# Kernel tuning notes

Measured on AMD Instinct MI355X. Metric: run time of the kernel, lower is better.

Reference implementation:

```python
import jax, jax.numpy as jnp
import numpy as np

N = 50000   # nodes
E = 800000  # edges (before self-loops)
IN = 128; H = 4; C = 32; HC = H * C; OUT = 47
EPS = 1e-16  # PyG softmax denominator eps
NEG_SLOPE = 0.2


def setup_inputs() -> dict:
    key = jax.random.key(0)
    ks = jax.random.split(key, 20)
    g = lambda k, shape, s=0.1: (jax.random.normal(k, shape, dtype=jnp.float32) * s)
    inp = {}
    inp["x"] = jax.random.normal(ks[0], (N, IN), dtype=jnp.float32)
    inp["edge_index"] = jax.random.randint(ks[1], (2, E), 0, N, dtype=jnp.int32)
    # layer 0: GATConv(IN -> H*C, concat=True) + skip Linear(IN -> HC)
    inp["lin_w0"] = g(ks[2], (IN, HC)); inp["att_src0"] = g(ks[3], (H, C)); inp["att_dst0"] = g(ks[4], (H, C))
    inp["bias0"] = g(ks[5], (HC,)); inp["skip_w0"] = g(ks[6], (IN, HC)); inp["skip_b0"] = g(ks[7], (HC,))
    # layer 1: GATConv(HC -> H*C, concat=True) + skip Linear(HC -> HC)
    inp["lin_w1"] = g(ks[8], (HC, HC)); inp["att_src1"] = g(ks[9], (H, C)); inp["att_dst1"] = g(ks[10], (H, C))
    inp["bias1"] = g(ks[11], (HC,)); inp["skip_w1"] = g(ks[12], (HC, HC)); inp["skip_b1"] = g(ks[13], (HC,))
    # layer 2: GATConv(HC -> OUT, heads=H, concat=False) + skip Linear(HC -> OUT)
    inp["lin_w2"] = g(ks[14], (HC, H * OUT)); inp["att_src2"] = g(ks[15], (H, OUT)); inp["att_dst2"] = g(ks[16], (H, OUT))
    inp["bias2"] = g(ks[17], (OUT,)); inp["skip_w2"] = g(ks[18], (HC, OUT)); inp["skip_b2"] = g(ks[19], (OUT,))
    return inp


def _gat_conv(x, src, dst, lin_w, att_src, att_dst, bias, concat):
    """PyG GATConv (self-loops already appended to src/dst)."""
    h, c = att_src.shape
    n = x.shape[0]
    xh = (x @ lin_w).reshape(n, h, c)                      # [N, H, C]
    a_src = jnp.einsum('nhc,hc->nh', xh, att_src)          # [N, H]
    a_dst = jnp.einsum('nhc,hc->nh', xh, att_dst)          # [N, H]
    e = a_src[src] + a_dst[dst]                            # [E', H]
    e = jax.nn.leaky_relu(e, NEG_SLOPE)
    # segment softmax over incoming edges per destination node
    m = jax.ops.segment_max(e, dst, num_segments=n)        # [N, H]
    ex = jnp.exp(e - m[dst])
    s = jax.ops.segment_sum(ex, dst, num_segments=n)       # [N, H]
    alpha = ex / (s[dst] + EPS)                            # [E', H]
    out = jax.ops.segment_sum(xh[src] * alpha[:, :, None], dst, num_segments=n)  # [N, H, C]
    out = out.reshape(n, h * c) if concat else out.mean(axis=1)
    return out + bias


def reference(x, edge_index, lin_w0, att_src0, att_dst0, bias0, skip_w0, skip_b0,
              lin_w1, att_src1, att_dst1, bias1, skip_w1, skip_b1,
              lin_w2, att_src2, att_dst2, bias2, skip_w2, skip_b2):
    n = x.shape[0]
    loop = jnp.arange(n, dtype=edge_index.dtype)
    src = jnp.concatenate([edge_index[0], loop])
    dst = jnp.concatenate([edge_index[1], loop])
    # layer 0 (+ skip, ELU; dropout is identity at inference)
    x = _gat_conv(x, src, dst, lin_w0, att_src0, att_dst0, bias0, True) + x @ skip_w0 + skip_b0
    x = jax.nn.elu(x)
    # layer 1
    x = _gat_conv(x, src, dst, lin_w1, att_src1, att_dst1, bias1, True) + x @ skip_w1 + skip_b1
    x = jax.nn.elu(x)
    # layer 2 (concat=False -> head mean), no activation
    x = _gat_conv(x, src, dst, lin_w2, att_src2, att_dst2, bias2, False) + x @ skip_w2 + skip_b2
    return x
```

## Files before the change

### kernel.cpp

```cpp
#include <hip/hip_runtime.h>
#include <math.h>
#include <type_traits>

#define KD 128
#define HC 128
#define NF2 188
#define NF2PB 192
#define OUTC 47

typedef __attribute__((ext_vector_type(8))) __bf16 bf16x8;
typedef __attribute__((ext_vector_type(4))) float f32x4;
typedef __attribute__((ext_vector_type(2))) float f32x2;

#ifdef __has_builtin
#if __has_builtin(__builtin_amdgcn_cvt_pk_f32_fp8)
#define HAVE_CVT_FP8_DEC 1
#endif
#if __has_builtin(__builtin_amdgcn_cvt_pk_fp8_f32)
#define HAVE_CVT_FP8_ENC 1
#endif
#endif

__device__ inline float bfhi_to_f(unsigned int u) {
    union { unsigned int u; float f; } c; c.u = u & 0xFFFF0000u; return c.f;
}
__device__ inline float bflo_to_f(unsigned int u) {
    union { unsigned int u; float f; } c; c.u = u << 16; return c.f;
}
__device__ inline unsigned short f_to_bfu(float f) {
    return __builtin_bit_cast(unsigned short, (__bf16)f);
}
__device__ inline unsigned int pk_bf(float a, float b) {
    return (unsigned int)f_to_bfu(a) | ((unsigned int)f_to_bfu(b) << 16);
}

__device__ inline void dot2bf(float& acc, unsigned int x, unsigned int a) {
    asm("v_dot2_f32_bf16 %0, %1, %2, %0" : "+v"(acc) : "v"(x), "v"(a));
}
__device__ inline unsigned int permb(unsigned int hi, unsigned int lo, unsigned int sel) {
    return __builtin_amdgcn_perm(hi, lo, sel);
}

#ifndef HAVE_CVT_FP8_DEC
__device__ inline float fp8_to_f32_b(unsigned int b) {
    int e = (b >> 3) & 15, m = b & 7;
    float v = e ? ldexpf((float)(8 + m), e - 10) : ldexpf((float)m, -9);
    return (b & 0x80) ? -v : v;
}
#endif
__device__ inline void fp8x4_dec(unsigned int q, float& a, float& b, float& c, float& d) {
#ifdef HAVE_CVT_FP8_DEC
    f32x2 lo = __builtin_amdgcn_cvt_pk_f32_fp8((int)q, false);
    f32x2 hi = __builtin_amdgcn_cvt_pk_f32_fp8((int)q, true);
    a = lo[0]; b = lo[1]; c = hi[0]; d = hi[1];
#else
    a = fp8_to_f32_b(q & 0xFF); b = fp8_to_f32_b((q >> 8) & 0xFF);
    c = fp8_to_f32_b((q >> 16) & 0xFF); d = fp8_to_f32_b((q >> 24) & 0xFF);
#endif
}
__device__ inline unsigned char f32_to_fp8(float v) {
#ifdef HAVE_CVT_FP8_ENC
    return (unsigned char)(__builtin_amdgcn_cvt_pk_fp8_f32(v, v, 0, false) & 0xFF);
#else
    unsigned u = __builtin_bit_cast(unsigned, v);
    unsigned s = (u >> 24) & 0x80;
    float a = fabsf(v);
    if (a < 0.0009765625f) return (unsigned char)s;
    if (a >= 448.f) return (unsigned char)(s | 0x7E);
    int e; float m = frexpf(a, &e);
    int E = e - 1 + 7;
    int mi = (int)rintf(m * 16.f);
    if (mi == 16) { mi = 8; ++E; if (E >= 16) return (unsigned char)(s | 0x7E); }
    if (E <= 0) {
        int q = (int)rintf(a * 512.f); if (q > 7) q = 7;
        return (unsigned char)(s | q);
    }
    return (unsigned char)(s | (E << 3) | (mi - 8));
#endif
}
__device__ inline float fp8dot(unsigned int q, float4 al, float acc) {
    float a, b, c, d;
    fp8x4_dec(q, a, b, c, d);
    return acc + al.x * a + al.y * b + al.z * c + al.w * d;
}

__global__ void count_kernel(const int* __restrict__ dst, int* deg, int e) {
    int t = blockIdx.x * blockDim.x + threadIdx.x;
    int base = t * 2;
    if (base + 1 < e) {
        int2 d = *(const int2*)(dst + base);
        atomicAdd(&deg[d.x], 1); atomicAdd(&deg[d.y], 1);
    } else {
        for (int k = base; k < e; ++k) atomicAdd(&deg[dst[k]], 1);
    }
}

__global__ __launch_bounds__(256) void scan_base_kernel(
    int* __restrict__ deg, int* counter,
    int* __restrict__ row_ptr, int* __restrict__ fill, int* __restrict__ col, int n) {
    int i = blockIdx.x * 256 + threadIdx.x;
    int v = (i < n) ? (deg[i] + 1) : 0;
    int lane = threadIdx.x & 63, w = threadIdx.x >> 6;
    int incl = v;
#pragma unroll
    for (int off = 1; off < 64; off <<= 1) {
        int u = __shfl_up(incl, off, 64);
        if (lane >= off) incl += u;
    }
    __shared__ int wsum[4];
    __shared__ int base_sh;
    if (lane == 63) wsum[w] = incl;
    __syncthreads();
    if (threadIdx.x == 0)
        base_sh = atomicAdd(counter, wsum[0] + wsum[1] + wsum[2] + wsum[3]);
    int woff = 0;
    for (int k = 0; k < w; ++k) woff += wsum[k];
    __syncthreads();
    int excl = base_sh + woff + incl - v;
    if (i < n) {
        row_ptr[i] = excl;
        col[excl] = i;
        fill[i] = excl + 1;
        deg[i] = v;
    }
}

__global__ void fill_kernel(const int* __restrict__ ei, int* fill, int* col, int e) {
    int t = blockIdx.x * blockDim.x + threadIdx.x;
    int base = t * 2;
    if (base + 1 < e) {
        int2 s = *(const int2*)(ei + base);
        int2 d = *(const int2*)(ei + e + base);
        int p0 = atomicAdd(&fill[d.x], 1);
        int p1 = atomicAdd(&fill[d.y], 1);
        __builtin_nontemporal_store(s.x, &col[p0]);
        __builtin_nontemporal_store(s.y, &col[p1]);
    } else {
        for (int k = base; k < e; ++k) {
            int pos = atomicAdd(&fill[ei[e + k]], 1);
            __builtin_nontemporal_store(ei[k], &col[pos]);
        }
    }
}

__global__ __launch_bounds__(256) void prep_w_kernel(
    const float* __restrict__ lw0, const float* __restrict__ sw0,
    const float* __restrict__ lw1, const float* __restrict__ sw1,
    const float* __restrict__ lw2, const float* __restrict__ sw2,
    __bf16* __restrict__ bt) {
    int idx = blockIdx.x * 256 + threadIdx.x;
    int buf = idx >> 15;
    int r = idx & 32767;
    int n = r >> 7, k = r & 127;
    float v = 0.f;
    if (buf == 0) v = (n < 128) ? lw0[k * 128 + n] : sw0[k * 128 + n - 128];
    else if (buf == 1) v = (n < 128) ? lw1[k * 128 + n] : sw1[k * 128 + n - 128];
    else {
        if (n < 188) v = lw2[k * 188 + n];
        else if (n >= 192 && n < 239) v = sw2[k * 47 + n - 192];
    }
    bt[idx] = (__bf16)v;
}

template <typename AT, typename SKT, int NLIN, int NSK, int TR>
__global__ __launch_bounds__(256) void gemm_fused_kernel(
    const AT* __restrict__ A, const __bf16* __restrict__ Bt,
    void* __restrict__ out0, int N0, int ldc0,
    const float* __restrict__ bias1, SKT* __restrict__ out1, int N1, int M) {
    __shared__ __bf16 As[64][136];
    __shared__ __bf16 Bs[64][136];
    int tid = threadIdx.x;
    int m0 = blockIdx.x * 64;

#pragma unroll
    for (int rep = 0; rep < 4; ++rep) {
        int idx = tid + rep * 256;
        int row = idx >> 4, seg = idx & 15;
        int gm = m0 + row;
        bf16x8 v = {};
        if (gm < M) {
            if constexpr (std::is_same<AT, float>::value) {
                const float* p = A + gm * KD + seg * 8;
                float4 f0 = *(const float4*)p;
                float4 f1 = *(const float4*)(p + 4);
                v[0] = (__bf16)f0.x; v[1] = (__bf16)f0.y; v[2] = (__bf16)f0.z; v[3] = (__bf16)f0.w;
                v[4] = (__bf16)f1.x; v[5] = (__bf16)f1.y; v[6] = (__bf16)f1.z; v[7] = (__bf16)f1.w;
            } else {
                v = *(const bf16x8*)(A + gm * KD + seg * 8);
            }
        }
        *(bf16x8*)&As[row][seg * 8] = v;
    }
    __syncthreads();

    int w = tid >> 6, lane = tid & 63;
    int lr = lane & 15, quad = lane >> 4;

#pragma unroll
    for (int t = 0; t < NLIN + NSK; ++t) {
        bool second = t >= NLIN;
        int N = second ? N1 : N0;
        int n0 = (second ? (t - NLIN) : t) * 64;
        if (t) __syncthreads();
#pragma unroll
        for (int rep = 0; rep < 4; ++rep) {
            int idx = tid + rep * 256;
            int row = idx >> 4, seg = idx & 15;
            *(bf16x8*)&Bs[row][seg * 8] =
                *(const bf16x8*)(Bt + ((t * 64 + row) << 7) + seg * 8);
        }
        __syncthreads();

        f32x4 acc[4] = {};
#pragma unroll
        for (int kc = 0; kc < 128; kc += 32) {
            bf16x8 a0 = *(const bf16x8*)&As[w * 16 + lr][kc + quad * 8];
            bf16x8 b0 = *(const bf16x8*)&Bs[lr][kc + quad * 8];
            bf16x8 b1 = *(const bf16x8*)&Bs[16 + lr][kc + quad * 8];
            bf16x8 b2 = *(const bf16x8*)&Bs[32 + lr][kc + quad * 8];
            bf16x8 b3 = *(const bf16x8*)&Bs[48 + lr][kc + quad * 8];
            acc[0] = __builtin_amdgcn_mfma_f32_16x16x32_bf16(a0, b0, acc[0], 0, 0, 0);
            acc[1] = __builtin_amdgcn_mfma_f32_16x16x32_bf16(a0, b1, acc[1], 0, 0, 0);
            acc[2] = __builtin_amdgcn_mfma_f32_16x16x32_bf16(a0, b2, acc[2], 0, 0, 0);
            acc[3] = __builtin_amdgcn_mfma_f32_16x16x32_bf16(a0, b3, acc[3], 0, 0, 0);
        }
#pragma unroll
        for (int c = 0; c < 4; ++c) {
#pragma unroll
            for (int reg = 0; reg < 4; ++reg) {
                int row = m0 + w * 16 + quad * 4 + reg;
                int colg = n0 + c * 16 + lr;
                if (row < M && colg < N) {
                    float v = acc[c][reg];
                    if (second) {
                        v += bias1[colg];
                        out1[row * N + colg] = (SKT)v;
                    } else if (TR) {
                        int h = (colg * 1395) >> 16;
                        ((unsigned char*)out0)[row * ldc0 + (colg - 47 * h) * 4 + h] =
                            f32_to_fp8(v);
                    } else {
                        ((__bf16*)out0)[row * ldc0 + colg] = (__bf16)v;
                    }
                }
            }
        }
    }
}

__global__ __launch_bounds__(256) void att_kernel(
    const __bf16* __restrict__ xh, const float* __restrict__ att_s,
    const float* __restrict__ att_d, float* __restrict__ a_src,
    float* __restrict__ a_dst, int n) {
    int tid = blockIdx.x * 256 + threadIdx.x;
    int node = tid >> 4;
    int l16 = threadIdx.x & 15;
    if (node >= n) return;
    uint4 q = ((const uint4*)xh)[node * 16 + l16];
    int f0 = l16 * 8;
    float4 as0 = *(const float4*)(att_s + f0);
    float4 as1 = *(const float4*)(att_s + f0 + 4);
    float4 ad0 = *(const float4*)(att_d + f0);
    float4 ad1 = *(const float4*)(att_d + f0 + 4);
    float x0 = bflo_to_f(q.x), x1 = bfhi_to_f(q.x);
    float x2 = bflo_to_f(q.y), x3 = bfhi_to_f(q.y);
    float x4 = bflo_to_f(q.z), x5 = bfhi_to_f(q.z);
    float x6 = bflo_to_f(q.w), x7 = bfhi_to_f(q.w);
    float hs = x0 * as0.x + x1 * as0.y + x2 * as0.z + x3 * as0.w
             + x4 * as1.x + x5 * as1.y + x6 * as1.z + x7 * as1.w;
    float hd = x0 * ad0.x + x1 * ad0.y + x2 * ad0.z + x3 * ad0.w
             + x4 * ad1.x + x5 * ad1.y + x6 * ad1.z + x7 * ad1.w;
    hs += __shfl_xor(hs, 1, 64); hs += __shfl_xor(hs, 2, 64);
    hd += __shfl_xor(hd, 1, 64); hd += __shfl_xor(hd, 2, 64);
    if ((l16 & 3) == 0) {
        int h = l16 >> 2;
        a_src[node * 4 + h] = hs;
        a_dst[node * 4 + h] = hd;
    }
}

__global__ __launch_bounds__(256) void att2_kernel(
    const unsigned char* __restrict__ xh8, const float* __restrict__ att_s,
    const float* __restrict__ att_d, float* __restrict__ a_src,
    float* __restrict__ a_dst, int n) {
    int node = (blockIdx.x * 256 + threadIdx.x) >> 6;
    int lane = threadIdx.x & 63;
    if (node >= n) return;
    float ps0 = 0.f, ps1 = 0.f, ps2 = 0.f, ps3 = 0.f;
    float pd0 = 0.f, pd1 = 0.f, pd2 = 0.f, pd3 = 0.f;
    if (lane < 47) {
        unsigned int q = ((const unsigned int*)(xh8 + node * NF2PB))[lane];
        float x0, x1, x2, x3;
        fp8x4_dec(q, x0, x1, x2, x3);
        ps0 = x0 * att_s[lane];       ps1 = x1 * att_s[47 + lane];
        ps2 = x2 * att_s[94 + lane];  ps3 = x3 * att_s[141 + lane];
        pd0 = x0 * att_d[lane];       pd1 = x1 * att_d[47 + lane];
        pd2 = x2 * att_d[94 + lane];  pd3 = x3 * att_d[141 + lane];
    }
#pragma unroll
    for (int off = 1; off <= 32; off <<= 1) {
        ps0 += __shfl_xor(ps0, off, 64); ps1 += __shfl_xor(ps1, off, 64);
        ps2 += __shfl_xor(ps2, off, 64); ps3 += __shfl_xor(ps3, off, 64);
        pd0 += __shfl_xor(pd0, off, 64); pd1 += __shfl_xor(pd1, off, 64);
        pd2 += __shfl_xor(pd2, off, 64); pd3 += __shfl_xor(pd3, off, 64);
    }
    if (lane < 4) {
        float vs = (lane == 0) ? ps0 : (lane == 1) ? ps1 : (lane == 2) ? ps2 : ps3;
        float vd = (lane == 0) ? pd0 : (lane == 1) ? pd1 : (lane == 2) ? pd2 : pd3;
        a_src[node * 4 + lane] = vs;
        a_dst[node * 4 + lane] = vd;
    }
}

template <int MODE>
__global__ __launch_bounds__(256) void agg_kernel(
    const void* __restrict__ xhp, const float* __restrict__ a_src,
    const float* __restrict__ a_dst, const void* __restrict__ skipp,
    const float* __restrict__ bias, const int* __restrict__ row_ptr,
    const int* __restrict__ deg, const int* __restrict__ col,
    void* __restrict__ outp, int n) {
    __shared__ float s_af[4][64][4];
    __shared__ unsigned s_ap[4][32][4];
    __shared__ int s_j[4][64];
    int w = threadIdx.x >> 6;
    int lane = threadIdx.x & 63;
    int node = (blockIdx.x << 2) + w;
    bool active = node < n;
    int node_c = active ? node : 0;
    int start = row_ptr[node_c];
    int end = start + (active ? deg[node_c] : 0);
    float4 ad4 = *(const float4*)(a_dst + 4 * node_c);
    float adh[4] = {ad4.x, ad4.y, ad4.z, ad4.w};

    int e0 = start + lane;
    bool ok0 = e0 < end;
    int jcap = ok0 ? col[e0] : 0;
    float evc[4];
    {
        float4 as4 = *(const float4*)(a_src + 4 * jcap);
        float v0 = as4.x + adh[0]; v0 = v0 > 0.f ? v0 : 0.2f * v0;
        float v1 = as4.y + adh[1]; v1 = v1 > 0.f ? v1 : 0.2f * v1;
        float v2 = as4.z + adh[2]; v2 = v2 > 0.f ? v2 : 0.2f * v2;
        float v3 = as4.w + adh[3]; v3 = v3 > 0.f ? v3 : 0.2f * v3;
        evc[0] = ok0 ? __expf(v0) : 0.f;
        evc[1] = ok0 ? __expf(v1) : 0.f;
        evc[2] = ok0 ? __expf(v2) : 0.f;
        evc[3] = ok0 ? __expf(v3) : 0.f;
    }
    float s[4] = {evc[0], evc[1], evc[2], evc[3]};
    for (int e = e0 + 64; e < end; e += 64) {
        int j = col[e];
        float4 as4 = *(const float4*)(a_src + 4 * j);
        float ev[4] = {as4.x + adh[0], as4.y + adh[1], as4.z + adh[2], as4.w + adh[3]};
#pragma unroll
        for (int h = 0; h < 4; ++h) {
            float v = ev[h] > 0.f ? ev[h] : 0.2f * ev[h];
            s[h] += __expf(v);
        }
    }
#pragma unroll
    for (int off = 32; off >= 1; off >>= 1)
#pragma unroll
        for (int h = 0; h < 4; ++h) s[h] += __shfl_xor(s[h], off, 64);
    float inv[4];
#pragma unroll
    for (int h = 0; h < 4; ++h) inv[h] = 1.f / (s[h] + 1e-16f);

    int half = lane >> 5, fl = lane & 31, myh2 = fl >> 3;
    bool lv = lane < 47;
    float acc0 = 0.f, acc1 = 0.f, acc2 = 0.f, acc3 = 0.f;
    const uint2* xb2 = (const uint2*)xhp;
    const unsigned int* x8 = (const unsigned int*)xhp;

    auto run_chunk = [&](int cnt) {
        if constexpr (MODE == 0) {
            int npair = (cnt + 1) >> 1;
            int p = half;
            for (; p + 2 < npair; p += 4) {
                int2 j0 = *(const int2*)&s_j[w][2 * p];
                int2 j1 = *(const int2*)&s_j[w][2 * p + 4];
                unsigned ap0 = s_ap[w][p][myh2];
                unsigned ap1 = s_ap[w][p + 2][myh2];
                uint2 qa0 = xb2[(j0.x << 5) + fl];
                uint2 qb0 = xb2[(j0.y << 5) + fl];
                uint2 qa1 = xb2[(j1.x << 5) + fl];
                uint2 qb1 = xb2[(j1.y << 5) + fl];
                dot2bf(acc0, permb(qb0.x, qa0.x, 0x05040100u), ap0);
                dot2bf(acc1, permb(qb0.x, qa0.x, 0x07060302u), ap0);
                dot2bf(acc2, permb(qb0.y, qa0.y, 0x05040100u), ap0);
                dot2bf(acc3, permb(qb0.y, qa0.y, 0x07060302u), ap0);
                dot2bf(acc0, permb(qb1.x, qa1.x, 0x05040100u), ap1);
                dot2bf(acc1, permb(qb1.x, qa1.x, 0x07060302u), ap1);
                dot2bf(acc2, permb(qb1.y, qa1.y, 0x05040100u), ap1);
                dot2bf(acc3, permb(qb1.y, qa1.y, 0x07060302u), ap1);
            }
            for (; p < npair; p += 2) {
                int2 j0 = *(const int2*)&s_j[w][2 * p];
                unsigned ap0 = s_ap[w][p][myh2];
                uint2 qa0 = xb2[(j0.x << 5) + fl];
                uint2 qb0 = xb2[(j0.y << 5) + fl];
                dot2bf(acc0, permb(qb0.x, qa0.x, 0x05040100u), ap0);
                dot2bf(acc1, permb(qb0.x, qa0.x, 0x07060302u), ap0);
                dot2bf(acc2, permb(qb0.y, qa0.y, 0x05040100u), ap0);
                dot2bf(acc3, permb(qb0.y, qa0.y, 0x07060302u), ap0);
            }
        } else {
            int t = 0;
            for (; t + 7 < cnt; t += 8) {
                unsigned int q0 = lv ? x8[s_j[w][t] * 48 + lane] : 0u;
                unsigned int q1 = lv ? x8[s_j[w][t + 1] * 48 + lane] : 0u;
                unsigned int q2 = lv ? x8[s_j[w][t + 2] * 48 + lane] : 0u;
                unsigned int q3 = lv ? x8[s_j[w][t + 3] * 48 + lane] : 0u;
                unsigned int q4 = lv ? x8[s_j[w][t + 4] * 48 + lane] : 0u;
                unsigned int q5 = lv ? x8[s_j[w][t + 5] * 48 + lane] : 0u;
                unsigned int q6 = lv ? x8[s_j[w][t + 6] * 48 + lane] : 0u;
                unsigned int q7 = lv ? x8[s_j[w][t + 7] * 48 + lane] : 0u;
                acc0 = fp8dot(q0, *(const float4*)&s_af[w][t][0], acc0);
                acc0 = fp8dot(q1, *(const float4*)&s_af[w][t + 1][0], acc0);
                acc0 = fp8dot(q2, *(const float4*)&s_af[w][t + 2][0], acc0);
                acc0 = fp8dot(q3, *(const float4*)&s_af[w][t + 3][0], acc0);
                acc0 = fp8dot(q4, *(const float4*)&s_af[w][t + 4][0], acc0);
                acc0 = fp8dot(q5, *(const float4*)&s_af[w][t + 5][0], acc0);
                acc0 = fp8dot(q6, *(const float4*)&s_af[w][t + 6][0], acc0);
                acc0 = fp8dot(q7, *(const float4*)&s_af[w][t + 7][0], acc0);
            }
            for (; t + 3 < cnt; t += 4) {
                unsigned int q0 = lv ? x8[s_j[w][t] * 48 + lane] : 0u;
                unsigned int q1 = lv ? x8[s_j[w][t + 1] * 48 + lane] : 0u;
                unsigned int q2 = lv ? x8[s_j[w][t + 2] * 48 + lane] : 0u;
                unsigned int q3 = lv ? x8[s_j[w][t + 3] * 48 + lane] : 0u;
                acc0 = fp8dot(q0, *(const float4*)&s_af[w][t][0], acc0);
                acc0 = fp8dot(q1, *(const float4*)&s_af[w][t + 1][0], acc0);
                acc0 = fp8dot(q2, *(const float4*)&s_af[w][t + 2][0], acc0);
                acc0 = fp8dot(q3, *(const float4*)&s_af[w][t + 3][0], acc0);
            }
            for (; t < cnt; ++t) {
                unsigned int q = lv ? x8[s_j[w][t] * 48 + lane] : 0u;
                acc0 = fp8dot(q, *(const float4*)&s_af[w][t][0], acc0);
            }
        }
    };

    {
        float al[4];
#pragma unroll
        for (int h = 0; h < 4; ++h) al[h] = evc[h] * inv[h];
        s_j[w][lane] = jcap;
        if constexpr (MODE == 0) {
            float o0 = __shfl_xor(al[0], 1, 64);
            float o1 = __shfl_xor(al[1], 1, 64);
            float o2 = __shfl_xor(al[2], 1, 64);
            float o3 = __shfl_xor(al[3], 1, 64);
            if (!(lane & 1)) {
                uint4 pk = make_uint4(pk_bf(al[0], o0), pk_bf(al[1], o1),
                                      pk_bf(al[2], o2), pk_bf(al[3], o3));
                *(uint4*)&s_ap[w][lane >> 1][0] = pk;
            }
        } else {
            *(float4*)&s_af[w][lane][0] = make_float4(al[0], al[1], al[2], al[3]);
        }
        int cnt = end - start; if (cnt > 64) cnt = 64;
        run_chunk(cnt);
    }
    for (int base = start + 64; base < end; base += 64) {
        int e = base + lane;
        bool ok = e < end;
        int jv = ok ? col[e] : 0;
        float4 as4 = *(const float4*)(a_src + 4 * jv);
        float asv[4] = {as4.x, as4.y, as4.z, as4.w};
        float al[4];
#pragma unroll
        for (int h = 0; h < 4; ++h) {
            float ev = asv[h] + adh[h];
            ev = ev > 0.f ? ev : 0.2f * ev;
            al[h] = ok ? __expf(ev) * inv[h] : 0.f;
        }
        s_j[w][lane] = jv;
        if constexpr (MODE == 0) {
            float o0 = __shfl_xor(al[0], 1, 64);
            float o1 = __shfl_xor(al[1], 1, 64);
            float o2 = __shfl_xor(al[2], 1, 64);
            float o3 = __shfl_xor(al[3], 1, 64);
            if (!(lane & 1)) {
                uint4 pk = make_uint4(pk_bf(al[0], o0), pk_bf(al[1], o1),
                                      pk_bf(al[2], o2), pk_bf(al[3], o3));
                *(uint4*)&s_ap[w][lane >> 1][0] = pk;
            }
        } else {
            *(float4*)&s_af[w][lane][0] = make_float4(al[0], al[1], al[2], al[3]);
        }
        int cnt = end - base; if (cnt > 64) cnt = 64;
        run_chunk(cnt);
    }

    if constexpr (MODE == 0) {
        acc0 += __shfl_xor(acc0, 32, 64);
        acc1 += __shfl_xor(acc1, 32, 64);
        acc2 += __shfl_xor(acc2, 32, 64);
        acc3 += __shfl_xor(acc3, 32, 64);
        if (active && half == 0) {
            float4 bb = *(const float4*)(bias + 4 * fl);
            uint2 skq = ((const uint2*)skipp)[(node << 5) + fl];
            float v0 = acc0 + bb.x + bflo_to_f(skq.x);
            float v1 = acc1 + bb.y + bfhi_to_f(skq.x);
            float v2 = acc2 + bb.z + bflo_to_f(skq.y);
            float v3 = acc3 + bb.w + bfhi_to_f(skq.y);
            v0 = v0 > 0.f ? v0 : (__expf(v0) - 1.f);
            v1 = v1 > 0.f ? v1 : (__expf(v1) - 1.f);
            v2 = v2 > 0.f ? v2 : (__expf(v2) - 1.f);
            v3 = v3 > 0.f ? v3 : (__expf(v3) - 1.f);
            uint2 o = make_uint2(pk_bf(v0, v1), pk_bf(v2, v3));
            ((uint2*)outp)[(node << 5) + fl] = o;
        }
    } else {
        if (active && lane < OUTC) {
            const float* skip = (const float*)skipp;
            float v = acc0 * 0.25f + bias[lane] + skip[node * OUTC + lane];
            ((float*)outp)[node * OUTC + lane] = v;
        }
    }
}

extern "C" void kernel_launch(void* const* d_in, const int* in_sizes, int n_in,
                              void* d_out, int out_size, void* d_ws, size_t ws_size,
                              hipStream_t stream) {
    const float* x        = (const float*)d_in[0];
    const int*   ei       = (const int*)d_in[1];
    const float* lin_w0   = (const float*)d_in[2];
    const float* att_src0 = (const float*)d_in[3];
    const float* att_dst0 = (const float*)d_in[4];
    const float* bias0    = (const float*)d_in[5];
    const float* skip_w0  = (const float*)d_in[6];
    const float* skip_b0  = (const float*)d_in[7];
    const float* lin_w1   = (const float*)d_in[8];
    const float* att_src1 = (const float*)d_in[9];
    const float* att_dst1 = (const float*)d_in[10];
    const float* bias1    = (const float*)d_in[11];
    const float* skip_w1  = (const float*)d_in[12];
    const float* skip_b1  = (const float*)d_in[13];
    const float* lin_w2   = (const float*)d_in[14];
    const float* att_src2 = (const float*)d_in[15];
    const float* att_dst2 = (const float*)d_in[16];
    const float* bias2    = (const float*)d_in[17];
    const float* skip_w2  = (const float*)d_in[18];
    const float* skip_b2  = (const float*)d_in[19];
    float* out = (float*)d_out;

    const int N = in_sizes[0] / KD;
    const int E = in_sizes[1] / 2;
    const int ET_ = E + N;

    char* ws = (char*)d_ws;
    size_t off = 0;
    auto alloc = [&](size_t bytes) -> void* {
        void* p = ws + off;
        off = (off + bytes + 255) & ~(size_t)255;
        return p;
    };
    void*   xh      = alloc((size_t)N * HC * 2 + 256);
    __bf16* buf_bf  = (__bf16*)alloc((size_t)N * HC * 2);
    void*   skipbuf = alloc((size_t)N * HC * 4);
    float* a_src    = (float*)alloc((size_t)N * 4 * 4);
    float* a_dst    = (float*)alloc((size_t)N * 4 * 4);
    int* deg        = (int*)alloc((size_t)N * 4);
    int* row_ptr    = (int*)alloc((size_t)N * 4);
    int* fill       = (int*)alloc((size_t)N * 4);
    int* col        = (int*)alloc((size_t)ET_ * 4);
    int* counter    = (int*)alloc(256);
    __bf16* Bt      = (__bf16*)alloc((size_t)3 * 256 * 128 * 2);

    prep_w_kernel<<<384, 256, 0, stream>>>(lin_w0, skip_w0, lin_w1, skip_w1,
                                           lin_w2, skip_w2, Bt);

    hipMemsetAsync(deg, 0, (size_t)N * 4, stream);
    hipMemsetAsync(counter, 0, 4, stream);
    count_kernel<<<(E / 2 + 255) / 256, 256, 0, stream>>>(ei + E, deg, E);
    scan_base_kernel<<<(N + 255) / 256, 256, 0, stream>>>(deg, counter, row_ptr, fill, col, N);
    fill_kernel<<<(E / 2 + 255) / 256, 256, 0, stream>>>(ei, fill, col, E);

    dim3 blk(256);
    int mblocks = (N + 63) / 64;
    int wave_blocks = (N + 3) / 4;
    int att_blocks = (N * 16 + 255) / 256;

    gemm_fused_kernel<float, __bf16, 2, 2, 0><<<mblocks, blk, 0, stream>>>(
        x, Bt, xh, HC, HC, skip_b0, (__bf16*)skipbuf, HC, N);
    att_kernel<<<att_blocks, blk, 0, stream>>>((const __bf16*)xh, att_src0, att_dst0,
                                               a_src, a_dst, N);
    agg_kernel<0><<<wave_blocks, blk, 0, stream>>>(xh, a_src, a_dst, skipbuf, bias0,
                                                   row_ptr, deg, col, buf_bf, N);
    gemm_fused_kernel<__bf16, __bf16, 2, 2, 0><<<mblocks, blk, 0, stream>>>(
        buf_bf, Bt + 32768, xh, HC, HC, skip_b1, (__bf16*)skipbuf, HC, N);
    att_kernel<<<att_blocks, blk, 0, stream>>>((const __bf16*)xh, att_src1, att_dst1,
                                               a_src, a_dst, N);
    agg_kernel<0><<<wave_blocks, blk, 0, stream>>>(xh, a_src, a_dst, skipbuf, bias1,
                                                   row_ptr, deg, col, buf_bf, N);
    gemm_fused_kernel<__bf16, float, 3, 1, 1><<<mblocks, blk, 0, stream>>>(
        buf_bf, Bt + 65536, xh, NF2, NF2PB, skip_b2, (float*)skipbuf, OUTC, N);
    att2_kernel<<<wave_blocks, blk, 0, stream>>>((const unsigned char*)xh, att_src2,
                                                 att_dst2, a_src, a_dst, N);
    agg_kernel<1><<<wave_blocks, blk, 0, stream>>>(xh, a_src, a_dst, skipbuf, bias2,
                                                   row_ptr, deg, col, out, N);
}
```

Before: 409.8 us.

## Partition CSR count and fill atomics by destination range across blocks

```diff
diff --git a/kernel.cpp b/kernel.cpp
--- a/kernel.cpp
+++ b/kernel.cpp
@@ -84,14 +84,28 @@
     return acc + al.x * a + al.y * b + al.z * c + al.w * d;
 }
 
-__global__ void count_kernel(const int* __restrict__ dst, int* deg, int e) {
-    int t = blockIdx.x * blockDim.x + threadIdx.x;
-    int base = t * 2;
-    if (base + 1 < e) {
-        int2 d = *(const int2*)(dst + base);
-        atomicAdd(&deg[d.x], 1); atomicAdd(&deg[d.y], 1);
+#define NPART 8
+#define EPB 2048
+
+__global__ __launch_bounds__(256) void count_kernel(
+    const int* __restrict__ dst, int* deg, int e, int rngsz) {
+    int r = blockIdx.x & (NPART - 1);
+    int chunk = blockIdx.x / NPART;
+    int base = chunk * EPB + threadIdx.x * 8;
+    int lo = r * rngsz, hi = lo + rngsz;
+    if (base >= e) return;
+    if (base + 7 < e) {
+        int4 d0 = *(const int4*)(dst + base);
+        int4 d1 = *(const int4*)(dst + base + 4);
+        int dd[8] = {d0.x, d0.y, d0.z, d0.w, d1.x, d1.y, d1.z, d1.w};
+#pragma unroll
+        for (int k = 0; k < 8; ++k)
+            if (dd[k] >= lo && dd[k] < hi) atomicAdd(&deg[dd[k]], 1);
     } else {
-        for (int k = base; k < e; ++k) atomicAdd(&deg[dst[k]], 1);
+        for (int k = base; k < e; ++k) {
+            int d = dst[k];
+            if (d >= lo && d < hi) atomicAdd(&deg[d], 1);
+        }
     }
 }
 
@@ -125,20 +139,32 @@
     }
 }
 
-__global__ void fill_kernel(const int* __restrict__ ei, int* fill, int* col, int e) {
-    int t = blockIdx.x * blockDim.x + threadIdx.x;
-    int base = t * 2;
-    if (base + 1 < e) {
-        int2 s = *(const int2*)(ei + base);
-        int2 d = *(const int2*)(ei + e + base);
-        int p0 = atomicAdd(&fill[d.x], 1);
-        int p1 = atomicAdd(&fill[d.y], 1);
-        __builtin_nontemporal_store(s.x, &col[p0]);
-        __builtin_nontemporal_store(s.y, &col[p1]);
+__global__ __launch_bounds__(256) void fill_kernel(
+    const int* __restrict__ ei, int* fill, int* col, int e, int rngsz) {
+    int r = blockIdx.x & (NPART - 1);
+    int chunk = blockIdx.x / NPART;
+    int base = chunk * EPB + threadIdx.x * 8;
+    int lo = r * rngsz, hi = lo + rngsz;
+    if (base >= e) return;
+    const int* dstp = ei + e;
+    if (base + 7 < e) {
+        int4 d0 = *(const int4*)(dstp + base);
+        int4 d1 = *(const int4*)(dstp + base + 4);
+        int dd[8] = {d0.x, d0.y, d0.z, d0.w, d1.x, d1.y, d1.z, d1.w};
+#pragma unroll
+        for (int k = 0; k < 8; ++k) {
+            if (dd[k] >= lo && dd[k] < hi) {
+                int pos = atomicAdd(&fill[dd[k]], 1);
+                col[pos] = ei[base + k];
+            }
+        }
     } else {
         for (int k = base; k < e; ++k) {
-            int pos = atomicAdd(&fill[ei[e + k]], 1);
-            __builtin_nontemporal_store(ei[k], &col[pos]);
+            int d = dstp[k];
+            if (d >= lo && d < hi) {
+                int pos = atomicAdd(&fill[d], 1);
+                col[pos] = ei[k];
+            }
         }
     }
 }
@@ -574,9 +600,11 @@
 
     hipMemsetAsync(deg, 0, (size_t)N * 4, stream);
     hipMemsetAsync(counter, 0, 4, stream);
-    count_kernel<<<(E / 2 + 255) / 256, 256, 0, stream>>>(ei + E, deg, E);
+    int rngsz = (N + NPART - 1) / NPART;
+    int cblocks = ((E + EPB - 1) / EPB) * NPART;
+    count_kernel<<<cblocks, 256, 0, stream>>>(ei + E, deg, E, rngsz);
     scan_base_kernel<<<(N + 255) / 256, 256, 0, stream>>>(deg, counter, row_ptr, fill, col, N);
-    fill_kernel<<<(E / 2 + 255) / 256, 256, 0, stream>>>(ei, fill, col, E);
+    fill_kernel<<<cblocks, 256, 0, stream>>>(ei, fill, col, E, rngsz);
 
     dim3 blk(256);
     int mblocks = (N + 63) / 64;
```

After: 392.5 us. 4.2% less time.
